# Performance work log

Measured on AMD Instinct MI355X. Metric: run time of the kernel, lower is better.

The kernel has to match this reference:

```python
import jax, jax.numpy as jnp
import numpy as np
from jax import lax

T, B, C, N, NKV, H = 4, 8, 256, 2048, 2048, 8
EPS = 1e-5
TAU = 2.0
ALPHA = 4.0  # spikingjelly Sigmoid surrogate default
SCALE = 0.125

@jax.custom_vjp
def spike(x):
    return (x >= 0.0).astype(x.dtype)

def _spike_fwd(x):
    return (x >= 0.0).astype(x.dtype), x

def _spike_bwd(x, g):
    s = jax.nn.sigmoid(ALPHA * x)
    return (g * ALPHA * s * (1.0 - s),)

spike.defvjp(_spike_fwd, _spike_bwd)

def lif(x, v_th):
    # x: [T, ...]; multi-step LIF: v += (x - v)/tau, fire at v_th, hard reset to 0 (detach_reset)
    def step(v, xt):
        v = v + (xt - v) / TAU
        s = spike(v - v_th)
        v = v * (1.0 - lax.stop_gradient(s))
        return v, s
    _, s = lax.scan(step, jnp.zeros_like(x[0]), x)
    return s

def bn_apply(x, p):
    # x: [M, C, L]; p: [4, C] = (gamma, beta, running_mean, running_var); inference BN
    g, b, mu, var = p
    inv = g / jnp.sqrt(var + EPS)
    return (x - mu[:, None]) * inv[:, None] + b[:, None]

def repconv(x, w1, p1, w3, w2, p2):
    # x: [M, C, L] -> [M, C, L]
    x = jnp.einsum('oc,mcl->mol', w1, x)  # 1x1 conv
    g, b, mu, var = p1
    inv = g / jnp.sqrt(var + EPS)
    x = (x - mu[:, None]) * inv[:, None] + b[:, None]
    pad = b - mu * inv  # BNAndPadLayer pad values [C]
    pad = jnp.broadcast_to(pad[None, :, None], (x.shape[0], x.shape[1], 1))
    x = jnp.concatenate([pad, x, pad], axis=2)
    # depthwise conv k=3, valid
    x = x[:, :, :-2] * w3[:, 0:1] + x[:, :, 1:-1] * w3[:, 1:2] + x[:, :, 2:] * w3[:, 2:3]
    x = jnp.einsum('oc,mcl->mol', w2, x)  # 1x1 conv
    return bn_apply(x, p2)

def _make_bn(key, n):
    k1, k2, k3, k4 = jax.random.split(key, 4)
    g = jax.random.uniform(k1, (n, C)) * 0.5 + 0.75
    b = jax.random.normal(k2, (n, C)) * 0.1
    mu = jax.random.normal(k3, (n, C)) * 0.1
    var = jax.random.uniform(k4, (n, C)) + 0.5
    return jnp.stack([g, b, mu, var], axis=1).astype(jnp.float32)  # [n, 4, C]

def setup_inputs():
    key = jax.random.key(0)
    ks = jax.random.split(key, 8)
    q = jax.random.normal(ks[0], (T, B, C, N), dtype=jnp.float32)
    k_ = jax.random.normal(ks[1], (T, B, C, NKV), dtype=jnp.float32)
    s1 = 1.0 / np.sqrt(C).astype(np.float32)
    rc_w1 = jax.random.normal(ks[2], (6, C, C), dtype=jnp.float32) * s1
    rc_w3 = jax.random.normal(ks[3], (6, C, 3), dtype=jnp.float32) * 0.3
    rc_w2 = jax.random.normal(ks[4], (6, C, C), dtype=jnp.float32) * s1
    rc_bn1 = _make_bn(ks[5], 6)
    rc_bn2 = _make_bn(ks[6], 6)
    out_bn = _make_bn(ks[7], 6)
    return {"q": q, "k_": k_, "rc_w1": rc_w1, "rc_bn1": rc_bn1, "rc_w3": rc_w3,
            "rc_w2": rc_w2, "rc_bn2": rc_bn2, "out_bn": out_bn}

def reference(q, k_, rc_w1, rc_bn1, rc_w3, rc_w2, rc_bn2, out_bn):
    Tt, Bb, Cc, Nn = q.shape
    hd = Cc // H

    def conv_bn(x, i):  # RepConv(i) followed by BatchNorm1d(i), over flattened (T*B)
        L = x.shape[-1]
        y = x.reshape(Tt * Bb, Cc, L)
        y = repconv(y, rc_w1[i], rc_bn1[i], rc_w3[i], rc_w2[i], rc_bn2[i])
        y = bn_apply(y, out_bn[i])
        return y.reshape(Tt, Bb, Cc, L)

    qf = conv_bn(q, 0)
    kf = conv_bn(conv_bn(k_, 1), 2)
    vf = conv_bn(conv_bn(k_, 3), 4)

    def to_heads(x):  # [T,B,C,L] -> [T,B,H,L,hd]
        L = x.shape[-1]
        return x.transpose(0, 1, 3, 2).reshape(Tt, Bb, L, H, hd).transpose(0, 1, 3, 2, 4)

    qh = to_heads(lif(qf, 1.0))
    kh = to_heads(lif(kf, 1.0))
    vh = to_heads(lif(vf, 1.0))
    kv = jnp.einsum('tbhnd,tbhne->tbhde', kh, vh)          # [T,B,H,hd,hd]
    a = jnp.einsum('tbhmd,tbhde->tbhme', qh, kv) * SCALE   # [T,B,H,N,hd]
    a = a.transpose(0, 1, 2, 4, 3).reshape(Tt, Bb, Cc, Nn)
    a = lif(a, 0.5)  # attn_lif, v_threshold=0.5
    return conv_bn(a, 5)
```

## Files before the change

### kernel.cpp

```cpp
#include <hip/hip_runtime.h>

#define C 256
#define NPOS 2048
#define BB 8
#define TTIME 4
#define PRM_STRIDE 132096
#define FRAG_ELEMS 196608

typedef float f32x4 __attribute__((ext_vector_type(4)));
typedef short short8 __attribute__((ext_vector_type(8)));
typedef unsigned int u32x4 __attribute__((ext_vector_type(4)));

static __device__ __forceinline__ unsigned short f2bf(float f) {
    unsigned int u = __float_as_uint(f);
    return (unsigned short)((u + 0x7FFFu + ((u >> 16) & 1u)) >> 16);
}
static __device__ __forceinline__ float bf2f(unsigned short b) {
    return __uint_as_float(((unsigned int)b) << 16);
}
static __device__ __forceinline__ void split3(float f, unsigned short& h,
                                              unsigned short& m, unsigned short& l) {
    h = f2bf(f);
    float r1 = f - bf2f(h);
    m = f2bf(r1);
    float r2 = r1 - bf2f(m);
    l = f2bf(r2);
}
static __device__ __forceinline__ unsigned long long pack4(const unsigned short* a) {
    return (unsigned long long)a[0] | ((unsigned long long)a[1] << 16)
         | ((unsigned long long)a[2] << 32) | ((unsigned long long)a[3] << 48);
}

__global__ __launch_bounds__(256) void prep_kern(
    const float* __restrict__ w1g, const float* __restrict__ bn1,
    const float* __restrict__ w3g, const float* __restrict__ w2g,
    const float* __restrict__ bn2, const float* __restrict__ bno,
    float* __restrict__ prm)
{
    int i = blockIdx.x;
    int tid = threadIdx.x;
    __shared__ float s1l[C], hcl[C], SGl[C];
    const float* b1 = bn1 + i * 4 * C;
    const float* b2 = bn2 + i * 4 * C;
    const float* bo = bno + i * 4 * C;
    float g1 = b1[tid], be1 = b1[C + tid], mu1 = b1[2 * C + tid], va1 = b1[3 * C + tid];
    float s1 = g1 / sqrtf(va1 + 1e-5f);
    float h1 = be1 - mu1 * s1;
    float g2 = b2[tid], be2 = b2[C + tid], mu2 = b2[2 * C + tid], va2 = b2[3 * C + tid];
    float s2 = g2 / sqrtf(va2 + 1e-5f);
    float h2 = be2 - mu2 * s2;
    float go = bo[tid], beo = bo[C + tid], muo = bo[2 * C + tid], vao = bo[3 * C + tid];
    float so = go / sqrtf(vao + 1e-5f);
    float ho = beo - muo * so;
    float SG = so * s2;
    float SH = so * h2 + ho;
    const float* w3i = w3g + i * C * 3;
    float w3s = w3i[tid * 3 + 0] + w3i[tid * 3 + 1] + w3i[tid * 3 + 2];
    s1l[tid] = s1; hcl[tid] = w3s * h1; SGl[tid] = SG;
    __syncthreads();
    float* prmi = prm + (size_t)i * PRM_STRIDE;
    const float* w1i = w1g + (size_t)i * C * C;
    const float* w2i = w2g + (size_t)i * C * C;
    for (int k = 0; k < C; ++k)
        prmi[tid * C + k] = s1l[k] * w1i[k * C + tid];
    for (int k = 0; k < C; ++k)
        prmi[65536 + tid * C + k] = SGl[k] * w2i[k * C + tid];
    for (int j = 0; j < 3; ++j)
        prmi[131072 + j * C + tid] = w3i[tid * 3 + j];
    float dot = 0.f;
    for (int k = 0; k < C; ++k)
        dot = fmaf(w2i[tid * C + k], hcl[k], dot);
    prmi[131840 + tid] = SG * dot + SH;
}

__global__ __launch_bounds__(256) void prep2_kern(
    const float* __restrict__ prm, unsigned short* __restrict__ frags)
{
    int b = blockIdx.x;
    int i = b >> 1, which = b & 1;
    const float* src = prm + (size_t)i * PRM_STRIDE + which * 65536;
    unsigned short* dst = frags + (size_t)b * FRAG_ELEMS;
    for (int e = threadIdx.x; e < 65536; e += 256) {
        int m = e & 255, k = e >> 8;
        float w = src[k * 256 + m];
        unsigned short h, mi, lo;
        split3(w, h, mi, lo);
        int ks = k >> 5, kin = k & 31;
        int mt = m >> 4;
        int lane = (m & 15) | (((kin >> 3) & 3) << 4);
        int j = kin & 7;
        size_t base = ((size_t)(ks * 16 + mt) * 3) * 64 * 8 + lane * 8 + j;
        dst[base] = h;
        dst[base + 512] = mi;
        dst[base + 1024] = lo;
    }
}

template<int IN_MODE, int OUT_T>
__global__ __launch_bounds__(256, 2) void conv_fused(
    const float* __restrict__ x, const unsigned int* __restrict__ xmask,
    float* __restrict__ y, const unsigned short* __restrict__ fragA,
    const unsigned short* __restrict__ fragB, const float* __restrict__ prmi)
{
    __shared__ __align__(16) char lds[30720];
    const int tid = threadIdx.x;
    const int lane = tid & 63, wv = tid >> 6;
    const int ctile = blockIdx.x & 31;
    const int slice = blockIdx.x >> 5;
    const int l0 = ctile * 64;
    const int lo4 = lane & 15, rg = lane >> 4;
    const int PA[6] = {0, 0, 1, 0, 2, 1};
    const int PB[6] = {0, 1, 0, 2, 0, 1};

    int mt[4];
#pragma unroll
    for (int rt = 0; rt < 4; ++rt) mt[rt] = wv + 4 * rt;

    f32x4 acc1[4][5];
#pragma unroll
    for (int a = 0; a < 4; ++a)
#pragma unroll
        for (int b = 0; b < 5; ++b) acc1[a][b] = (f32x4)0.f;

    const short8* Ab1 = (const short8*)fragA;

    float LDf[20];
    unsigned int LDu[20];

#define ISSUE(sp_)                                                             \
    {                                                                          \
        _Pragma("unroll")                                                      \
        for (int it = 0; it < 5; ++it) {                                       \
            int u = it * 256 + tid;                                            \
            int col = u % 80;                                                  \
            int kq4 = u / 80;                                                  \
            int gpos = l0 - 8 + col;                                           \
            bool ok = (unsigned)gpos < (unsigned)NPOS;                         \
            int k0 = (sp_) * 64 + kq4 * 4;                                     \
            if (IN_MODE == 2) {                                                \
                const unsigned int* mg = xmask + (size_t)slice * C * 64 + (gpos >> 5); \
                _Pragma("unroll")                                              \
                for (int j = 0; j < 4; ++j)                                    \
                    LDu[it * 4 + j] = ok ? mg[(k0 + j) * 64] : 0u;             \
            } else if (IN_MODE == 0) {                                         \
                const float* xg = x + (size_t)slice * C * NPOS + gpos;         \
                _Pragma("unroll")                                              \
                for (int j = 0; j < 4; ++j)                                    \
                    LDf[it * 4 + j] = ok ? xg[(size_t)(k0 + j) * NPOS] : 0.f;  \
            } else {                                                           \
                if (ok) {                                                      \
                    float4 a4 = *(const float4*)(x + ((size_t)slice * NPOS + gpos) * C + k0); \
                    LDf[it * 4 + 0] = a4.x; LDf[it * 4 + 1] = a4.y;            \
                    LDf[it * 4 + 2] = a4.z; LDf[it * 4 + 3] = a4.w;            \
                } else {                                                       \
                    _Pragma("unroll")                                          \
                    for (int j = 0; j < 4; ++j) LDf[it * 4 + j] = 0.f;         \
                }                                                              \
            }                                                                  \
        }                                                                      \
    }

#define SPLIT(sp_)                                                             \
    {                                                                          \
        _Pragma("unroll")                                                      \
        for (int it = 0; it < 5; ++it) {                                       \
            int u = it * 256 + tid;                                            \
            int col = u % 80;                                                  \
            int kq4 = u / 80;                                                  \
            int base = col * 128 + ((((kq4 >> 1) ^ (col & 7)) & 7) << 4) + (kq4 & 1) * 8; \
            if (IN_MODE == 2) {                                                \
                int gpos = l0 - 8 + col;                                       \
                int bitp = gpos & 31;                                          \
                unsigned short th[4];                                          \
                _Pragma("unroll")                                              \
                for (int j = 0; j < 4; ++j)                                    \
                    th[j] = ((LDu[it * 4 + j] >> bitp) & 1u) ? 0x3F80 : 0;     \
                *(unsigned long long*)(lds + base) = pack4(th);                \
            } else {                                                           \
                unsigned short th[4], tm_[4], tl_[4];                          \
                _Pragma("unroll")                                              \
                for (int j = 0; j < 4; ++j)                                    \
                    split3(LDf[it * 4 + j], th[j], tm_[j], tl_[j]);            \
                *(unsigned long long*)(lds + base) = pack4(th);                \
                *(unsigned long long*)(lds + 10240 + base) = pack4(tm_);       \
                *(unsigned long long*)(lds + 20480 + base) = pack4(tl_);       \
            }                                                                  \
        }                                                                      \
    }

    ISSUE(0);
#pragma unroll
    for (int sp = 0; sp < 4; ++sp) {
        SPLIT(sp);
        if (sp < 3) ISSUE(sp + 1);
        __syncthreads();
#pragma unroll
        for (int ksl = 0; ksl < 2; ++ksl) {
            int ks = sp * 2 + ksl;
            int oct = ksl * 4 + rg;
            short8 A[4][3];
#pragma unroll
            for (int rt = 0; rt < 4; ++rt)
#pragma unroll
                for (int s = 0; s < 3; ++s)
                    A[rt][s] = Ab1[(size_t)((ks * 16 + mt[rt]) * 3 + s) * 64 + lane];
            int ba[5];
#pragma unroll
            for (int ct = 0; ct < 5; ++ct) {
                int colb = ct * 16 + lo4;
                ba[ct] = colb * 128 + (((oct ^ (colb & 7)) & 7) << 4);
            }
            if (IN_MODE == 2) {
                short8 B[5];
#pragma unroll
                for (int ct = 0; ct < 5; ++ct)
                    B[ct] = *(const short8*)(lds + ba[ct]);
                __builtin_amdgcn_s_setprio(1);
#pragma unroll
                for (int pp = 0; pp < 3; ++pp)
#pragma unroll
                    for (int rt = 0; rt < 4; ++rt)
#pragma unroll
                        for (int ct = 0; ct < 5; ++ct)
                            acc1[rt][ct] = __builtin_amdgcn_mfma_f32_16x16x32_bf16(
                                A[rt][pp], B[ct], acc1[rt][ct], 0, 0, 0);
                __builtin_amdgcn_s_setprio(0);
            } else {
                short8 B[5][3];
#pragma unroll
                for (int ct = 0; ct < 5; ++ct) {
                    B[ct][0] = *(const short8*)(lds + ba[ct]);
                    B[ct][1] = *(const short8*)(lds + 10240 + ba[ct]);
                    B[ct][2] = *(const short8*)(lds + 20480 + ba[ct]);
                }
                __builtin_amdgcn_s_setprio(1);
#pragma unroll
                for (int pp = 0; pp < 6; ++pp)
#pragma unroll
                    for (int rt = 0; rt < 4; ++rt)
#pragma unroll
                        for (int ct = 0; ct < 5; ++ct)
                            acc1[rt][ct] = __builtin_amdgcn_mfma_f32_16x16x32_bf16(
                                A[rt][PA[pp]], B[ct][PB[pp]], acc1[rt][ct], 0, 0, 0);
                __builtin_amdgcn_s_setprio(0);
            }
        }
        __syncthreads();
    }

    const float* w3p = prmi + 131072;
    const short8* Ab2 = (const short8*)fragB;
    f32x4 acc2[4][4];
#pragma unroll
    for (int a = 0; a < 4; ++a)
#pragma unroll
        for (int b = 0; b < 4; ++b) acc2[a][b] = (f32x4)0.f;

#pragma unroll
    for (int s = 0; s < 4; ++s) {
        {
            const int rt = s;
            int RTB = mt[rt] << 4;
            float w3a[4], w3b[4], w3c[4];
#pragma unroll
            for (int r = 0; r < 4; ++r) {
                int m = RTB + rg * 4 + r;
                w3a[r] = w3p[m]; w3b[r] = w3p[256 + m]; w3c[r] = w3p[512 + m];
            }
            int k0 = (RTB & 63) + rg * 4;
#pragma unroll
            for (int ct = 0; ct < 5; ++ct) {
                int sc = ct * 16 + lo4;
                unsigned short th[4], tm_[4], tl_[4];
#pragma unroll
                for (int r = 0; r < 4; ++r) {
                    float cur = acc1[rt][ct][r];
                    float prevv = acc1[rt][ct > 0 ? ct - 1 : 0][r];
                    float nextv = acc1[rt][ct < 4 ? ct + 1 : 4][r];
                    float sL  = __shfl(cur, lane - 1);
                    float sL2 = __shfl(prevv, lane + 15);
                    float sR  = __shfl(cur, lane + 1);
                    float sR2 = __shfl(nextv, lane - 15);
                    float uL = lo4 ? sL : sL2;
                    float uR = (lo4 == 15) ? sR2 : sR;
                    float t = w3a[r] * uL + w3b[r] * cur + w3c[r] * uR;
                    split3(t, th[r], tm_[r], tl_[r]);
                }
                if (sc >= 8 && sc < 72) {
                    int oc = sc - 8;
                    int base = oc * 128 + ((((k0 >> 3) ^ (oc & 7)) & 7) << 4) + (k0 & 7) * 2;
                    *(unsigned long long*)(lds + base) = pack4(th);
                    *(unsigned long long*)(lds + 8192 + base) = pack4(tm_);
                    *(unsigned long long*)(lds + 16384 + base) = pack4(tl_);
                }
            }
        }
        __syncthreads();
#pragma unroll
        for (int ksl = 0; ksl < 2; ++ksl) {
            int ks = s * 2 + ksl;
            int chunk = ksl * 4 + rg;
            short8 A[4][3];
#pragma unroll
            for (int rt = 0; rt < 4; ++rt)
#pragma unroll
                for (int ss = 0; ss < 3; ++ss)
                    A[rt][ss] = Ab2[(size_t)((ks * 16 + mt[rt]) * 3 + ss) * 64 + lane];
            short8 B[4][3];
#pragma unroll
            for (int ct = 0; ct < 4; ++ct) {
                int oc = ct * 16 + lo4;
                int ba = oc * 128 + (((chunk ^ (oc & 7)) & 7) << 4);
                B[ct][0] = *(const short8*)(lds + ba);
                B[ct][1] = *(const short8*)(lds + 8192 + ba);
                B[ct][2] = *(const short8*)(lds + 16384 + ba);
            }
            __builtin_amdgcn_s_setprio(1);
#pragma unroll
            for (int pp = 0; pp < 6; ++pp)
#pragma unroll
                for (int rt = 0; rt < 4; ++rt)
#pragma unroll
                    for (int ct = 0; ct < 4; ++ct)
                        acc2[rt][ct] = __builtin_amdgcn_mfma_f32_16x16x32_bf16(
                            A[rt][PA[pp]], B[ct][PB[pp]], acc2[rt][ct], 0, 0, 0);
            __builtin_amdgcn_s_setprio(0);
        }
        __syncthreads();
    }

    const float* bs = prmi + 131840;
    float* yS = y + (size_t)slice * NPOS * C;
    if (OUT_T) {
#pragma unroll
        for (int ph = 0; ph < 4; ++ph) {
            if (ph) __syncthreads();
#pragma unroll
            for (int rt = 0; rt < 4; ++rt) {
                int m0 = (mt[rt] << 4) + rg * 4;
                int chunk = (mt[rt] << 2) + rg;
                int cl = lo4;
                f32x4 o;
#pragma unroll
                for (int r = 0; r < 4; ++r) o[r] = acc2[rt][ph][r] + bs[m0 + r];
                *(f32x4*)(lds + cl * 1024 + ((chunk ^ (cl & 7)) << 4)) = o;
            }
            __syncthreads();
#pragma unroll
            for (int i = 0; i < 4; ++i) {
                int u = i * 256 + tid;
                int cl = u >> 6, cchunk = u & 63;
                f32x4 o = *(const f32x4*)(lds + cl * 1024 + ((cchunk ^ (cl & 7)) << 4));
                int pos = l0 + ph * 16 + cl;
                *(f32x4*)(yS + (size_t)pos * C + cchunk * 4) = o;
            }
        }
    } else {
#pragma unroll
        for (int rt = 0; rt < 4; ++rt) {
            int m0 = (mt[rt] << 4) + rg * 4;
#pragma unroll
            for (int ct = 0; ct < 4; ++ct) {
                int pos = l0 + ct * 16 + lo4;
#pragma unroll
                for (int r = 0; r < 4; ++r)
                    yS[(size_t)(m0 + r) * NPOS + pos] = acc2[rt][ct][r] + bs[m0 + r];
            }
        }
    }
#undef ISSUE
#undef SPLIT
}

__global__ __launch_bounds__(256) void lif_kern(
    const float* __restrict__ yT, unsigned int* __restrict__ mask, float vth)
{
    int g = blockIdx.x * 256 + threadIdx.x;
    int ch = g & 255;
    int w = (g >> 8) & 63;
    int b = g >> 14;
    float v[32];
#pragma unroll
    for (int j = 0; j < 32; ++j) v[j] = 0.f;
    for (int t = 0; t < TTIME; ++t) {
        int slice = t * BB + b;
        const float* yr = yT + ((size_t)slice * NPOS + w * 32) * C + ch;
        unsigned int mw = 0;
#pragma unroll
        for (int j = 0; j < 32; ++j) {
            float yy = yr[(size_t)j * C];
            float vn = v[j] + (yy - v[j]) * 0.5f;
            int sp = (vn - vth) >= 0.0f;
            mw |= ((unsigned int)sp) << j;
            v[j] = sp ? 0.f : vn;
        }
        mask[((size_t)slice * C + ch) * 64 + w] = mw;
    }
}

__global__ __launch_bounds__(256) void kv_kern(
    const unsigned int* __restrict__ km_g, const unsigned int* __restrict__ vm_g,
    int* __restrict__ kv_g)
{
    int blk = blockIdx.x;
    int h = blk & 7;
    int tb = blk >> 3;
    __shared__ unsigned int km[32][65], vm[32][65];
    int tid = threadIdx.x;
#pragma unroll
    for (int i = 0; i < 8; ++i) {
        int idx = i * 256 + tid;
        int d = idx >> 6, w = idx & 63;
        size_t rb = ((size_t)tb * C + h * 32 + d) * 64 + w;
        km[d][w] = km_g[rb];
        vm[d][w] = vm_g[rb];
    }
    __syncthreads();
#pragma unroll
    for (int k = 0; k < 4; ++k) {
        int p = k * 256 + tid;
        int d = p >> 5, e = p & 31;
        int s = 0;
#pragma unroll
        for (int w = 0; w < 64; ++w)
            s += __popc(km[d][w] & vm[e][w]);
        kv_g[(size_t)blk * 1024 + p] = s;
    }
}

__global__ __launch_bounds__(256) void attn_kern(
    const unsigned int* __restrict__ qm_g, const int* __restrict__ kv_g,
    unsigned int* __restrict__ amask)
{
    int blk = blockIdx.x;
    int chunk = blk & 7;
    int bh = blk >> 3;
    int h = bh & 7, b = bh >> 3;
    int tid = threadIdx.x;
    __shared__ int kvs[1024];
    __shared__ unsigned int qw[32][8];
    float v[32];
#pragma unroll
    for (int e = 0; e < 32; ++e) v[e] = 0.f;
    for (int t = 0; t < TTIME; ++t) {
        int tb = t * BB + b;
        __syncthreads();
#pragma unroll
        for (int k = 0; k < 4; ++k)
            kvs[k * 256 + tid] = kv_g[((size_t)tb * 8 + h) * 1024 + k * 256 + tid];
        {
            int d = tid >> 3, wi = tid & 7;
            qw[d][wi] = qm_g[((size_t)tb * C + h * 32 + d) * 64 + chunk * 8 + wi];
        }
        __syncthreads();
        int a[32];
#pragma unroll
        for (int e = 0; e < 32; ++e) a[e] = 0;
        int wsel = tid >> 5, bitp = tid & 31;
        for (int d = 0; d < 32; ++d) {
            if ((qw[d][wsel] >> bitp) & 1u) {
                const int* kr = &kvs[d * 32];
#pragma unroll
                for (int e = 0; e < 32; ++e) a[e] += kr[e];
            }
        }
#pragma unroll
        for (int e = 0; e < 32; ++e) {
            float f = (float)a[e] * 0.125f;
            v[e] = v[e] + (f - v[e]) * 0.5f;
            int sp = (v[e] - 0.5f) >= 0.0f;
            unsigned long long bb = __ballot(sp);
            if ((tid & 63) == 0) {
                int ch = h * 32 + e;
                unsigned long long* dst = (unsigned long long*)amask
                    + ((size_t)tb * C + ch) * 32 + chunk * 4 + (tid >> 6);
                *dst = bb;
            }
            if (sp) v[e] = 0.f;
        }
    }
}

extern "C" void kernel_launch(void* const* d_in, const int* in_sizes, int n_in,
                              void* d_out, int out_size, void* d_ws, size_t ws_size,
                              hipStream_t stream) {
    const float* q   = (const float*)d_in[0];
    const float* k_  = (const float*)d_in[1];
    const float* w1g = (const float*)d_in[2];
    const float* bn1 = (const float*)d_in[3];
    const float* w3g = (const float*)d_in[4];
    const float* w2g = (const float*)d_in[5];
    const float* bn2 = (const float*)d_in[6];
    const float* bno = (const float*)d_in[7];

    float* prm = (float*)d_ws;
    unsigned short* frags = (unsigned short*)(prm + 6 * PRM_STRIDE);
    float* bufA = (float*)(frags + 12 * FRAG_ELEMS);
    float* bufB = bufA + 16777216;
    unsigned int* qmask = (unsigned int*)(bufB + 16777216);
    unsigned int* kmask = qmask + 524288;
    unsigned int* vmask = kmask + 524288;
    int* kvb = (int*)(vmask + 524288);
    unsigned int* amask = (unsigned int*)(kvb + 262144);

    prep_kern<<<6, 256, 0, stream>>>(w1g, bn1, w3g, w2g, bn2, bno, prm);
    prep2_kern<<<12, 256, 0, stream>>>(prm, frags);

#define FRAG(i, which) (frags + (size_t)((i) * 2 + (which)) * FRAG_ELEMS)
#define PRMI(i) (prm + (size_t)(i) * PRM_STRIDE)

    conv_fused<0, 1><<<1024, 256, 0, stream>>>(q, nullptr, bufA, FRAG(0, 0), FRAG(0, 1), PRMI(0));
    lif_kern<<<512, 256, 0, stream>>>(bufA, qmask, 1.0f);
    conv_fused<0, 1><<<1024, 256, 0, stream>>>(k_, nullptr, bufA, FRAG(1, 0), FRAG(1, 1), PRMI(1));
    conv_fused<1, 1><<<1024, 256, 0, stream>>>(bufA, nullptr, bufB, FRAG(2, 0), FRAG(2, 1), PRMI(2));
    lif_kern<<<512, 256, 0, stream>>>(bufB, kmask, 1.0f);
    conv_fused<0, 1><<<1024, 256, 0, stream>>>(k_, nullptr, bufA, FRAG(3, 0), FRAG(3, 1), PRMI(3));
    conv_fused<1, 1><<<1024, 256, 0, stream>>>(bufA, nullptr, bufB, FRAG(4, 0), FRAG(4, 1), PRMI(4));
    lif_kern<<<512, 256, 0, stream>>>(bufB, vmask, 1.0f);

    kv_kern<<<256, 256, 0, stream>>>(kmask, vmask, kvb);
    attn_kern<<<512, 256, 0, stream>>>(qmask, kvb, amask);

    conv_fused<2, 0><<<1024, 256, 0, stream>>>(nullptr, amask, (float*)d_out, FRAG(5, 0), FRAG(5, 1), PRMI(5));
}
```

Measured before the change: 819.4 us.

## Double-buffer LDS staging in both conv GEMM stages to halve barriers

Doubles the shared-memory buffers for the input tile and the depthwise-output tile. Each stage now splits or writes the next chunk into the alternate buffer after issuing the current chunk's MFMAs, so one __syncthreads per iteration replaces two. The aim is to overlap conversion and LDS writes with matrix work and to cut barrier stalls. LDS use doubles to 60 KB per block, which may limit occupancy under launch_bounds(256,2).

```diff
diff --git a/kernel.cpp b/kernel.cpp
--- a/kernel.cpp
+++ b/kernel.cpp
@@ -102,7 +102,7 @@
     float* __restrict__ y, const unsigned short* __restrict__ fragA,
     const unsigned short* __restrict__ fragB, const float* __restrict__ prmi)
 {
-    __shared__ __align__(16) char lds[30720];
+    __shared__ __align__(16) char lds[61440];
     const int tid = threadIdx.x;
     const int lane = tid & 63, wv = tid >> 6;
     const int ctile = blockIdx.x & 31;
@@ -111,6 +111,8 @@
     const int lo4 = lane & 15, rg = lane >> 4;
     const int PA[6] = {0, 0, 1, 0, 2, 1};
     const int PB[6] = {0, 1, 0, 2, 0, 1};
+    const int XBUFSZ = (IN_MODE == 2) ? 10240 : 30720;
+    const int TBUFSZ = 24576;
 
     int mt[4];
 #pragma unroll
@@ -160,14 +162,14 @@
         }                                                                      \
     }
 
-#define SPLIT(sp_)                                                             \
+#define SPLIT(xb_)                                                             \
     {                                                                          \
         _Pragma("unroll")                                                      \
         for (int it = 0; it < 5; ++it) {                                       \
             int u = it * 256 + tid;                                            \
             int col = u % 80;                                                  \
             int kq4 = u / 80;                                                  \
-            int base = col * 128 + ((((kq4 >> 1) ^ (col & 7)) & 7) << 4) + (kq4 & 1) * 8; \
+            int base = (xb_) + col * 128 + ((((kq4 >> 1) ^ (col & 7)) & 7) << 4) + (kq4 & 1) * 8; \
             if (IN_MODE == 2) {                                                \
                 int gpos = l0 - 8 + col;                                       \
                 int bitp = gpos & 31;                                          \
@@ -189,11 +191,12 @@
     }
 
     ISSUE(0);
+    SPLIT(0);
+    ISSUE(1);
+    __syncthreads();
 #pragma unroll
     for (int sp = 0; sp < 4; ++sp) {
-        SPLIT(sp);
-        if (sp < 3) ISSUE(sp + 1);
-        __syncthreads();
+        const int xb = (sp & 1) * XBUFSZ;
 #pragma unroll
         for (int ksl = 0; ksl < 2; ++ksl) {
             int ks = sp * 2 + ksl;
@@ -208,7 +211,7 @@
 #pragma unroll
             for (int ct = 0; ct < 5; ++ct) {
                 int colb = ct * 16 + lo4;
-                ba[ct] = colb * 128 + (((oct ^ (colb & 7)) & 7) << 4);
+                ba[ct] = xb + colb * 128 + (((oct ^ (colb & 7)) & 7) << 4);
             }
             if (IN_MODE == 2) {
                 short8 B[5];
@@ -245,6 +248,8 @@
                 __builtin_amdgcn_s_setprio(0);
             }
         }
+        if (sp < 3) SPLIT(((sp + 1) & 1) * XBUFSZ);
+        if (sp < 2) ISSUE(sp + 2);
         __syncthreads();
     }
 
@@ -256,46 +261,50 @@
 #pragma unroll
         for (int b = 0; b < 4; ++b) acc2[a][b] = (f32x4)0.f;
 
+#define DWSPLIT(s_, tb_)                                                       \
+    {                                                                          \
+        const int rt = (s_);                                                   \
+        int RTB = mt[rt] << 4;                                                 \
+        float w3a[4], w3b[4], w3c[4];                                          \
+        _Pragma("unroll")                                                      \
+        for (int r = 0; r < 4; ++r) {                                          \
+            int m = RTB + rg * 4 + r;                                          \
+            w3a[r] = w3p[m]; w3b[r] = w3p[256 + m]; w3c[r] = w3p[512 + m];     \
+        }                                                                      \
+        int k0 = (RTB & 63) + rg * 4;                                          \
+        _Pragma("unroll")                                                      \
+        for (int ct = 0; ct < 5; ++ct) {                                       \
+            int sc = ct * 16 + lo4;                                            \
+            unsigned short th[4], tm_[4], tl_[4];                              \
+            _Pragma("unroll")                                                  \
+            for (int r = 0; r < 4; ++r) {                                      \
+                float cur = acc1[rt][ct][r];                                   \
+                float prevv = acc1[rt][ct > 0 ? ct - 1 : 0][r];                \
+                float nextv = acc1[rt][ct < 4 ? ct + 1 : 4][r];                \
+                float sL  = __shfl(cur, lane - 1);                             \
+                float sL2 = __shfl(prevv, lane + 15);                          \
+                float sR  = __shfl(cur, lane + 1);                             \
+                float sR2 = __shfl(nextv, lane - 15);                          \
+                float uL = lo4 ? sL : sL2;                                     \
+                float uR = (lo4 == 15) ? sR2 : sR;                             \
+                float t = w3a[r] * uL + w3b[r] * cur + w3c[r] * uR;            \
+                split3(t, th[r], tm_[r], tl_[r]);                              \
+            }                                                                  \
+            if (sc >= 8 && sc < 72) {                                          \
+                int oc = sc - 8;                                               \
+                int base = (tb_) + oc * 128 + ((((k0 >> 3) ^ (oc & 7)) & 7) << 4) + (k0 & 7) * 2; \
+                *(unsigned long long*)(lds + base) = pack4(th);                \
+                *(unsigned long long*)(lds + 8192 + base) = pack4(tm_);        \
+                *(unsigned long long*)(lds + 16384 + base) = pack4(tl_);       \
+            }                                                                  \
+        }                                                                      \
+    }
+
+    DWSPLIT(0, 0);
+    __syncthreads();
 #pragma unroll
     for (int s = 0; s < 4; ++s) {
-        {
-            const int rt = s;
-            int RTB = mt[rt] << 4;
-            float w3a[4], w3b[4], w3c[4];
-#pragma unroll
-            for (int r = 0; r < 4; ++r) {
-                int m = RTB + rg * 4 + r;
-                w3a[r] = w3p[m]; w3b[r] = w3p[256 + m]; w3c[r] = w3p[512 + m];
-            }
-            int k0 = (RTB & 63) + rg * 4;
-#pragma unroll
-            for (int ct = 0; ct < 5; ++ct) {
-                int sc = ct * 16 + lo4;
-                unsigned short th[4], tm_[4], tl_[4];
-#pragma unroll
-                for (int r = 0; r < 4; ++r) {
-                    float cur = acc1[rt][ct][r];
-                    float prevv = acc1[rt][ct > 0 ? ct - 1 : 0][r];
-                    float nextv = acc1[rt][ct < 4 ? ct + 1 : 4][r];
-                    float sL  = __shfl(cur, lane - 1);
-                    float sL2 = __shfl(prevv, lane + 15);
-                    float sR  = __shfl(cur, lane + 1);
-                    float sR2 = __shfl(nextv, lane - 15);
-                    float uL = lo4 ? sL : sL2;
-                    float uR = (lo4 == 15) ? sR2 : sR;
-                    float t = w3a[r] * uL + w3b[r] * cur + w3c[r] * uR;
-                    split3(t, th[r], tm_[r], tl_[r]);
-                }
-                if (sc >= 8 && sc < 72) {
-                    int oc = sc - 8;
-                    int base = oc * 128 + ((((k0 >> 3) ^ (oc & 7)) & 7) << 4) + (k0 & 7) * 2;
-                    *(unsigned long long*)(lds + base) = pack4(th);
-                    *(unsigned long long*)(lds + 8192 + base) = pack4(tm_);
-                    *(unsigned long long*)(lds + 16384 + base) = pack4(tl_);
-                }
-            }
-        }
-        __syncthreads();
+        const int tb = (s & 1) * TBUFSZ;
 #pragma unroll
         for (int ksl = 0; ksl < 2; ++ksl) {
             int ks = s * 2 + ksl;
@@ -310,7 +319,7 @@
 #pragma unroll
             for (int ct = 0; ct < 4; ++ct) {
                 int oc = ct * 16 + lo4;
-                int ba = oc * 128 + (((chunk ^ (oc & 7)) & 7) << 4);
+                int ba = tb + oc * 128 + (((chunk ^ (oc & 7)) & 7) << 4);
                 B[ct][0] = *(const short8*)(lds + ba);
                 B[ct][1] = *(const short8*)(lds + 8192 + ba);
                 B[ct][2] = *(const short8*)(lds + 16384 + ba);
@@ -326,8 +335,12 @@
                             A[rt][PA[pp]], B[ct][PB[pp]], acc2[rt][ct], 0, 0, 0);
             __builtin_amdgcn_s_setprio(0);
         }
+        if (s == 0) DWSPLIT(1, TBUFSZ);
+        if (s == 1) DWSPLIT(2, 0);
+        if (s == 2) DWSPLIT(3, TBUFSZ);
         __syncthreads();
     }
+#undef DWSPLIT
 
     const float* bs = prmi + 131840;
     float* yS = y + (size_t)slice * NPOS * C;
```

Result: no change. 814.9 us (-0.5%).
